# Kernel tuning notes

Hardware: AMD Instinct MI355X
Metric: run time of the kernel (lower is better)

## Reference

```python
import jax, jax.numpy as jnp
import numpy as np


def _lstm_cell(x, h, c, Wih, Whh, b):
    # torch gate order: input, forget, cell(g), output
    gates = x @ Wih.T + h @ Whh.T + b  # [B, 4H]
    i, f, g, o = jnp.split(gates, 4, axis=-1)
    i = jax.nn.sigmoid(i)
    f = jax.nn.sigmoid(f)
    g = jnp.tanh(g)
    o = jax.nn.sigmoid(o)
    c = f * c + i * g
    return o * jnp.tanh(c), c


def setup_inputs() -> dict:
    key = jax.random.key(0)
    ks = jax.random.split(key, 20)
    B, Te, Td, X, H = 4096, 168, 24, 8, 64
    s = 0.1  # weight scale for numerical sanity in the AR sampling loop
    return {
        "enc_x": jax.random.normal(ks[0], (B, Te, X), jnp.float32),
        "enc_z": jax.random.uniform(ks[1], (B, Te, 1), jnp.float32),
        "dec_x": jax.random.normal(ks[2], (B, Td, X - 1), jnp.float32),
        "v": jax.random.uniform(ks[3], (B, 1, 1), jnp.float32) + 0.5,  # positive scale
        "eps": jax.random.normal(ks[4], (B, Td, 1), jnp.float32),
        "W_ih0": s * jax.random.normal(ks[5], (4 * H, X), jnp.float32),
        "W_hh0": s * jax.random.normal(ks[6], (4 * H, H), jnp.float32),
        "b0": s * jax.random.normal(ks[7], (4 * H,), jnp.float32),
        "W_ih1": s * jax.random.normal(ks[8], (4 * H, H), jnp.float32),
        "W_hh1": s * jax.random.normal(ks[9], (4 * H, H), jnp.float32),
        "b1": s * jax.random.normal(ks[10], (4 * H,), jnp.float32),
        "W_ih2": s * jax.random.normal(ks[11], (4 * H, H), jnp.float32),
        "W_hh2": s * jax.random.normal(ks[12], (4 * H, H), jnp.float32),
        "b2": s * jax.random.normal(ks[13], (4 * H,), jnp.float32),
        "w_m": s * jax.random.normal(ks[14], (H, 1), jnp.float32),
        "b_m": jnp.zeros((1,), jnp.float32),
        "w_a": s * jax.random.normal(ks[15], (H, 1), jnp.float32),
        "b_a": jnp.zeros((1,), jnp.float32),
    }


def reference(enc_x, enc_z, dec_x, v, eps,
              W_ih0, W_hh0, b0, W_ih1, W_hh1, b1, W_ih2, W_hh2, b2,
              w_m, b_m, w_a, b_a):
    B = enc_x.shape[0]
    H = W_hh0.shape[1]

    def step3(x, h, c):
        h0, c0 = _lstm_cell(x, h[0], c[0], W_ih0, W_hh0, b0)
        h1, c1 = _lstm_cell(h0, h[1], c[1], W_ih1, W_hh1, b1)
        h2, c2 = _lstm_cell(h1, h[2], c[2], W_ih2, W_hh2, b2)
        return (h0, h1, h2), (c0, c1, c2), h2

    z0 = jnp.zeros((B, H), enc_x.dtype)
    h = (z0, z0, z0)
    c = (z0, z0, z0)

    # ---- encoder: 3-layer LSTM over Te steps ----
    def enc_step(carry, x_t):
        h, c = carry
        h, c, _ = step3(x_t, h, c)
        return (h, c), None

    (h, c), _ = jax.lax.scan(enc_step, (h, c), jnp.swapaxes(enc_x, 0, 1))

    vf = v[:, 0, :]                 # [B, 1]
    z = enc_z[:, -1, :] / vf        # [B, 1]

    def dec_step(carry, inp):
        h, c, z = carry
        x_t, e_t = inp              # [B, X-1], [B, 1]
        x = jnp.concatenate([z, x_t], axis=-1)   # [B, X]
        h, c, o = step3(x, h, c)
        m = (o @ w_m + b_m) * vf                  # Gaussian mean, rescaled
        a = jax.nn.softplus(o @ w_a + b_a) * vf   # Gaussian std, rescaled
        zs = m + a * e_t                          # reparameterized sample
        return (h, c, zs / vf), zs

    xs = (jnp.swapaxes(dec_x, 0, 1), jnp.swapaxes(eps, 0, 1))
    _, Z = jax.lax.scan(dec_step, (h, c, z), xs)  # [Td, B, 1]
    return jnp.swapaxes(Z, 0, 1)                  # [B, Td, 1]
```

## Files before the change

kernel.cpp:

```cpp
#include <hip/hip_runtime.h>
#include <math.h>

#define B_TOT 4096
#define TE 168
#define TD 24
#define NWG 256
#define HSTR 72

typedef _Float16 f16;
typedef __attribute__((ext_vector_type(8))) _Float16 f16x8;
typedef __attribute__((ext_vector_type(4))) float f32x4;

#define SCL_S (-1.4426950408889634f)
#define SCL_G (2.885390081777927f)

__global__ __launch_bounds__(256) void pack_kernel(
    const float* __restrict__ Wih0, const float* __restrict__ Whh0,
    const float* __restrict__ Wih1, const float* __restrict__ Whh1,
    const float* __restrict__ Wih2, const float* __restrict__ Whh2,
    f16* __restrict__ pk)
{
    int idx = blockIdx.x * 256 + threadIdx.x;
    int j = idx & 7;
    int t = idx >> 3;
    int ln = t & 63; t >>= 6;
    int c  = t & 3;  t >>= 2;
    int q  = t & 3;  t >>= 2;
    int l  = t % 3;
    int w  = t / 3;
    int row = q * 64 + w * 16 + (ln & 15);
    int k   = c * 32 + ((ln >> 4) << 3) + j;
    float val = 0.f;
    if (l == 0) {
        if (k < 8)                 val = Wih0[row * 8 + k];
        else if (k >= 32 && k < 96) val = Whh0[row * 64 + (k - 32)];
    } else if (l == 1) {
        val = (k < 64) ? Wih1[row * 64 + k] : Whh1[row * 64 + (k - 64)];
    } else {
        val = (k < 64) ? Wih2[row * 64 + k] : Whh2[row * 64 + (k - 64)];
    }
    const float sc = (q == 2) ? SCL_G : SCL_S;
    pk[idx] = (f16)(val * sc);
}

__device__ __forceinline__ float softplusf(float x) { return fmaxf(x, 0.f) + log1pf(__expf(-fabsf(x))); }

__global__ __launch_bounds__(256, 1) void lstm_kernel(
    const float* __restrict__ enc_x, const float* __restrict__ enc_z,
    const float* __restrict__ dec_x, const float* __restrict__ v,
    const float* __restrict__ eps,   const f16* __restrict__ pk,
    const float* __restrict__ b0, const float* __restrict__ b1,
    const float* __restrict__ b2,
    const float* __restrict__ w_m, const float* __restrict__ b_m,
    const float* __restrict__ w_a, const float* __restrict__ b_a,
    float* __restrict__ out)
{
    const int tid  = threadIdx.x;
    const int lane = tid & 63;
    const int wv   = tid >> 6;
    const int bg   = blockIdx.x * 16;
    const int m16  = lane & 15;
    const int quad = lane >> 4;

    __shared__ f16  hbuf[2][3][16][HSTR];
    __shared__ f16  xbuf[16][32];
    __shared__ float zbuf[16];

    {
        uint* hz = (uint*)&hbuf[0][0][0][0];
        const int HW = 2 * 3 * 16 * HSTR / 2;
        for (int i = tid; i < HW; i += 256) hz[i] = 0u;
        ((uint*)&xbuf[0][0])[tid] = 0u;
    }

    f16x8 wgt[3][4][4];
#pragma unroll
    for (int l = 0; l < 3; ++l)
#pragma unroll
        for (int q = 0; q < 4; ++q)
#pragma unroll
            for (int c = 0; c < 4; ++c) {
                if (l == 0 && c == 3) continue;
                size_t off = (((((size_t)wv * 3 + l) * 4 + q) * 4 + c) * 64 + lane) * 8;
                wgt[l][q][c] = *(const f16x8*)(pk + off);
            }

    const int hid_self = wv * 16 + m16;
    f32x4 bsp[3][4];
#pragma unroll
    for (int q = 0; q < 4; ++q) {
        const float sc = (q == 2) ? SCL_G : SCL_S;
        float v0 = b0[q * 64 + hid_self] * sc;
        float v1 = b1[q * 64 + hid_self] * sc;
        float v2 = b2[q * 64 + hid_self] * sc;
        bsp[0][q] = (f32x4){v0, v0, v0, v0};
        bsp[1][q] = (f32x4){v1, v1, v1, v1};
        bsp[2][q] = (f32x4){v2, v2, v2, v2};
    }

    f16* hb = &hbuf[0][0][0][0];
    const int aoff = m16 * HSTR + quad * 8;
    float cst[3][4] = {};

#define HBASE(pp, l) (hb + ((pp) * 3 + (l)) * (16 * HSTR))
#define MFMA16(af, bf, cf) __builtin_amdgcn_mfma_f32_16x16x32_f16(af, bf, cf, 0, 0, 0)

#define MM_F(P, aptr, l, c)                                                   \
    {                                                                         \
        f16x8 af = *(const f16x8*)(aptr);                                     \
        P##0 = MFMA16(af, wgt[l][0][c], bsp[l][0]);                           \
        P##1 = MFMA16(af, wgt[l][1][c], bsp[l][1]);                           \
        P##2 = MFMA16(af, wgt[l][2][c], bsp[l][2]);                           \
        P##3 = MFMA16(af, wgt[l][3][c], bsp[l][3]);                           \
    }
#define MM(P, aptr, l, c)                                                     \
    {                                                                         \
        f16x8 af = *(const f16x8*)(aptr);                                     \
        P##0 = MFMA16(af, wgt[l][0][c], P##0);                                \
        P##1 = MFMA16(af, wgt[l][1][c], P##1);                                \
        P##2 = MFMA16(af, wgt[l][2][c], P##2);                                \
        P##3 = MFMA16(af, wgt[l][3][c], P##3);                                \
    }

#define CELL(P, l, PP)                                                        \
    {                                                                         \
        f16* hw = HBASE(PP, l) + hid_self;                                    \
        _Pragma("unroll")                                                     \
        for (int r = 0; r < 4; ++r) {                                         \
            float iv = __builtin_amdgcn_rcpf(1.f + __builtin_amdgcn_exp2f(P##0[r])); \
            float fv = __builtin_amdgcn_rcpf(1.f + __builtin_amdgcn_exp2f(P##1[r])); \
            float gv = fmaf(-2.f, __builtin_amdgcn_rcpf(1.f + __builtin_amdgcn_exp2f(P##2[r])), 1.f); \
            float ov = __builtin_amdgcn_rcpf(1.f + __builtin_amdgcn_exp2f(P##3[r])); \
            float cn = fmaf(fv, cst[l][r], iv * gv);                          \
            cst[l][r] = cn;                                                   \
            float tc = fmaf(-2.f, __builtin_amdgcn_rcpf(1.f + __builtin_amdgcn_exp2f(cn * SCL_G)), 1.f); \
            hw[(quad * 4 + r) * HSTR] = (f16)(ov * tc);                       \
        }                                                                     \
    }

    const int  mS   = tid >> 3, kS = tid & 7;
    const bool isst = tid < 128;

#define ENC_STEP(PP, t)                                                       \
    {                                                                         \
        __syncthreads();                       \
        f32x4 ac0, ac1, ac2, ac3, bc0, bc1, bc2, bc3;                         \
        MM_F(ac, &xbuf[0][0] + m16 * 32 + quad * 8, 0, 0);                    \
        MM_F(bc, HBASE(1 - (PP), 1) + aoff, 1, 2);                            \
        MM(ac, HBASE(1 - (PP), 0) + aoff, 0, 1);                              \
        MM(bc, HBASE(1 - (PP), 1) + aoff + 32, 1, 3);                         \
        MM(ac, HBASE(1 - (PP), 0) + aoff + 32, 0, 2);                         \
        CELL(ac, 0, PP);                                                      \
        __syncthreads();                    \
        if (isst && (t) + 1 < TE) {                                           \
            xbuf[mS][kS] = (f16)xpre;                                         \
            if ((t) + 2 < TE)                                                 \
                xpre = enc_x[((size_t)(bg + mS) * TE + (t) + 2) * 8 + kS];    \
        }                                                                     \
        MM_F(ac, HBASE(1 - (PP), 2) + aoff, 2, 2);                            \
        MM(bc, HBASE(PP, 0) + aoff, 1, 0);                                    \
        MM(ac, HBASE(1 - (PP), 2) + aoff + 32, 2, 3);                         \
        MM(bc, HBASE(PP, 0) + aoff + 32, 1, 1);                               \
        CELL(bc, 1, PP);                                                      \
        __syncthreads();                               \
        MM(ac, HBASE(PP, 1) + aoff, 2, 0);                                    \
        MM(ac, HBASE(PP, 1) + aoff + 32, 2, 1);                               \
        CELL(ac, 2, PP);                                                      \
    }

    __syncthreads();

    float xpre = 0.f;
    if (isst) {
        xbuf[mS][kS] = (f16)enc_x[((size_t)(bg + mS) * TE + 0) * 8 + kS];
        xpre = enc_x[((size_t)(bg + mS) * TE + 1) * 8 + kS];
    }
    for (int t = 0; t < TE; t += 2) {
        ENC_STEP(0, t)
        ENC_STEP(1, t + 1)
    }

    const int   mH = tid >> 4;
    const float vf = v[bg + mH];
    float wmr[4], war[4];
#pragma unroll
    for (int r = 0; r < 4; ++r) {
        wmr[r] = w_m[(tid & 15) + 16 * r];
        war[r] = w_a[(tid & 15) + 16 * r];
    }
    const float bmv = b_m[0], bav = b_a[0];
    if ((tid & 15) == 0) zbuf[mH] = enc_z[(size_t)(bg + mH) * TE + (TE - 1)] / vf;

#define DEC_STEP(PP, t)                                                       \
    {                                                                         \
        __syncthreads();                        \
        if (isst) {                                                           \
            float xv = (kS == 0) ? zbuf[mS]                                   \
                                 : dec_x[((size_t)(bg + mS) * TD + (t)) * 7 + (kS - 1)]; \
            xbuf[mS][kS] = (f16)xv;                                           \
        }                                                                     \
        __syncthreads();                                \
        f32x4 ac0, ac1, ac2, ac3, bc0, bc1, bc2, bc3;                         \
        MM_F(ac, &xbuf[0][0] + m16 * 32 + quad * 8, 0, 0);                    \
        MM_F(bc, HBASE(1 - (PP), 1) + aoff, 1, 2);                            \
        MM(ac, HBASE(1 - (PP), 0) + aoff, 0, 1);                              \
        MM(bc, HBASE(1 - (PP), 1) + aoff + 32, 1, 3);                         \
        MM(ac, HBASE(1 - (PP), 0) + aoff + 32, 0, 2);                         \
        CELL(ac, 0, PP);                                                      \
        __syncthreads();                                               \
        MM_F(ac, HBASE(1 - (PP), 2) + aoff, 2, 2);                            \
        MM(bc, HBASE(PP, 0) + aoff, 1, 0);                                    \
        MM(ac, HBASE(1 - (PP), 2) + aoff + 32, 2, 3);                         \
        MM(bc, HBASE(PP, 0) + aoff + 32, 1, 1);                               \
        CELL(bc, 1, PP);                                                      \
        __syncthreads();                                               \
        MM(ac, HBASE(PP, 1) + aoff, 2, 0);                                    \
        MM(ac, HBASE(PP, 1) + aoff + 32, 2, 1);                               \
        CELL(ac, 2, PP);                                                      \
        __syncthreads();                               \
        {                                                                     \
            float sm = 0.f, sa = 0.f;                                         \
            const f16* h2p = HBASE(PP, 2) + mH * HSTR;                        \
            _Pragma("unroll")                                                 \
            for (int r = 0; r < 4; ++r) {                                     \
                float hv = (float)h2p[(tid & 15) + 16 * r];                   \
                sm += hv * wmr[r];                                            \
                sa += hv * war[r];                                            \
            }                                                                 \
            _Pragma("unroll")                                                 \
            for (int off = 1; off < 16; off <<= 1) {                          \
                sm += __shfl_xor(sm, off, 64);                                \
                sa += __shfl_xor(sa, off, 64);                                \
            }                                                                 \
            if ((tid & 15) == 0) {                                            \
                float mo  = (sm + bmv) * vf;                                  \
                float ao  = softplusf(sa + bav) * vf;                         \
                float zsv = mo + ao * eps[(size_t)(bg + mH) * TD + (t)];      \
                out[(size_t)(bg + mH) * TD + (t)] = zsv;                      \
                zbuf[mH] = zsv / vf;                                          \
            }                                                                 \
        }                                                                     \
    }

    for (int t = 0; t < TD; t += 2) {
        DEC_STEP(0, t)
        DEC_STEP(1, t + 1)
    }

#undef HBASE
#undef MFMA16
#undef MM_F
#undef MM
#undef CELL
#undef ENC_STEP
#undef DEC_STEP
}

extern "C" void kernel_launch(void* const* d_in, const int* in_sizes, int n_in,
                              void* d_out, int out_size, void* d_ws, size_t ws_size,
                              hipStream_t stream) {
    const float* enc_x = (const float*)d_in[0];
    const float* enc_z = (const float*)d_in[1];
    const float* dec_x = (const float*)d_in[2];
    const float* v     = (const float*)d_in[3];
    const float* eps   = (const float*)d_in[4];
    const float* Wih0  = (const float*)d_in[5];
    const float* Whh0  = (const float*)d_in[6];
    const float* b0    = (const float*)d_in[7];
    const float* Wih1  = (const float*)d_in[8];
    const float* Whh1  = (const float*)d_in[9];
    const float* b1    = (const float*)d_in[10];
    const float* Wih2  = (const float*)d_in[11];
    const float* Whh2  = (const float*)d_in[12];
    const float* b2    = (const float*)d_in[13];
    const float* w_m   = (const float*)d_in[14];
    const float* b_m   = (const float*)d_in[15];
    const float* w_a   = (const float*)d_in[16];
    const float* b_a   = (const float*)d_in[17];
    float* out = (float*)d_out;
    f16*   pk  = (f16*)d_ws;

    pack_kernel<<<384, 256, 0, stream>>>(Wih0, Whh0, Wih1, Whh1, Wih2, Whh2, pk);
    lstm_kernel<<<NWG, 256, 0, stream>>>(enc_x, enc_z, dec_x, v, eps, pk,
                                         b0, b1, b2, w_m, b_m, w_a, b_a, out);
}
```

Before: 364.9 us.

## Wavefront-pipeline encoder layers across timesteps and merge sigmoid/tanh reciprocals

The encoder now runs as a diagonal wavefront. In each round, layer 0 handles step t, layer 1 step t-1 and layer 2 step t-2, so a single barrier per round replaces three per step. Prologue and epilogue rounds fill and drain the pipeline, x is double-buffered, and the decoder's buffer parity is adjusted to match the skewed hidden-state layout. The cell math also combines pairs of reciprocals (i·g and o·tanh(c)) into one rcp each, which shortens the transcendental chain. The trade-off is more live accumulator registers per round and possible overflow in the merged products for large gate pre-activations.

```diff
diff --git a/kernel.cpp b/kernel.cpp
--- a/kernel.cpp
+++ b/kernel.cpp
@@ -63,14 +63,15 @@
     const int quad = lane >> 4;
 
     __shared__ f16  hbuf[2][3][16][HSTR];
-    __shared__ f16  xbuf[16][32];
+    __shared__ f16  xbuf[2][16][32];
     __shared__ float zbuf[16];
 
     {
         uint* hz = (uint*)&hbuf[0][0][0][0];
         const int HW = 2 * 3 * 16 * HSTR / 2;
         for (int i = tid; i < HW; i += 256) hz[i] = 0u;
-        ((uint*)&xbuf[0][0])[tid] = 0u;
+        uint* xz = (uint*)&xbuf[0][0][0];
+        for (int i = tid; i < 512; i += 256) xz[i] = 0u;
     }
 
     f16x8 wgt[3][4][4];
@@ -127,58 +128,70 @@
         f16* hw = HBASE(PP, l) + hid_self;                                    \
         _Pragma("unroll")                                                     \
         for (int r = 0; r < 4; ++r) {                                         \
-            float iv = __builtin_amdgcn_rcpf(1.f + __builtin_amdgcn_exp2f(P##0[r])); \
-            float fv = __builtin_amdgcn_rcpf(1.f + __builtin_amdgcn_exp2f(P##1[r])); \
-            float gv = fmaf(-2.f, __builtin_amdgcn_rcpf(1.f + __builtin_amdgcn_exp2f(P##2[r])), 1.f); \
-            float ov = __builtin_amdgcn_rcpf(1.f + __builtin_amdgcn_exp2f(P##3[r])); \
-            float cn = fmaf(fv, cst[l][r], iv * gv);                          \
+            float Ei = __builtin_amdgcn_exp2f(P##0[r]);                       \
+            float Ef = __builtin_amdgcn_exp2f(P##1[r]);                       \
+            float Eg = __builtin_amdgcn_exp2f(P##2[r]);                       \
+            float Eo = __builtin_amdgcn_exp2f(P##3[r]);                       \
+            float fv  = __builtin_amdgcn_rcpf(1.f + Ef);                      \
+            float Rig = __builtin_amdgcn_rcpf((1.f + Ei) * (1.f + Eg));       \
+            float cn  = fmaf(fv, cst[l][r], (Eg - 1.f) * Rig);                \
             cst[l][r] = cn;                                                   \
-            float tc = fmaf(-2.f, __builtin_amdgcn_rcpf(1.f + __builtin_amdgcn_exp2f(cn * SCL_G)), 1.f); \
-            hw[(quad * 4 + r) * HSTR] = (f16)(ov * tc);                       \
+            float Ec  = __builtin_amdgcn_exp2f(cn * SCL_G);                   \
+            float Roc = __builtin_amdgcn_rcpf((1.f + Eo) * (1.f + Ec));       \
+            hw[(quad * 4 + r) * HSTR] = (f16)((Ec - 1.f) * Roc);              \
         }                                                                     \
     }
 
     const int  mS   = tid >> 3, kS = tid & 7;
     const bool isst = tid < 128;
 
-#define ENC_STEP(PP, t)                                                       \
-    {                                                                         \
-        __syncthreads();                       \
-        f32x4 ac0, ac1, ac2, ac3, bc0, bc1, bc2, bc3;                         \
-        MM_F(ac, &xbuf[0][0] + m16 * 32 + quad * 8, 0, 0);                    \
-        MM_F(bc, HBASE(1 - (PP), 1) + aoff, 1, 2);                            \
-        MM(ac, HBASE(1 - (PP), 0) + aoff, 0, 1);                              \
-        MM(bc, HBASE(1 - (PP), 1) + aoff + 32, 1, 3);                         \
-        MM(ac, HBASE(1 - (PP), 0) + aoff + 32, 0, 2);                         \
-        CELL(ac, 0, PP);                                                      \
-        __syncthreads();                    \
-        if (isst && (t) + 1 < TE) {                                           \
-            xbuf[mS][kS] = (f16)xpre;                                         \
-            if ((t) + 2 < TE)                                                 \
-                xpre = enc_x[((size_t)(bg + mS) * TE + (t) + 2) * 8 + kS];    \
-        }                                                                     \
-        MM_F(ac, HBASE(1 - (PP), 2) + aoff, 2, 2);                            \
-        MM(bc, HBASE(PP, 0) + aoff, 1, 0);                                    \
-        MM(ac, HBASE(1 - (PP), 2) + aoff + 32, 2, 3);                         \
-        MM(bc, HBASE(PP, 0) + aoff + 32, 1, 1);                               \
-        CELL(bc, 1, PP);                                                      \
-        __syncthreads();                               \
-        MM(ac, HBASE(PP, 1) + aoff, 2, 0);                                    \
-        MM(ac, HBASE(PP, 1) + aoff + 32, 2, 1);                               \
-        CELL(ac, 2, PP);                                                      \
+#define ROUND(PP, D0, D1, D2, DS, DP, T0)                                     \
+    {                                                                         \
+        __syncthreads();                                                      \
+        f32x4 a00, a01, a02, a03, a10, a11, a12, a13, a20, a21, a22, a23;     \
+        if (D0) {                                                             \
+            MM_F(a0, &xbuf[PP][0][0] + m16 * 32 + quad * 8, 0, 0);            \
+            MM(a0, HBASE(1 - (PP), 0) + aoff,      0, 1);                     \
+            MM(a0, HBASE(1 - (PP), 0) + aoff + 32, 0, 2);                     \
+        }                                                                     \
+        if (D1) {                                                             \
+            MM_F(a1, HBASE(1 - (PP), 0) + aoff,      1, 0);                   \
+            MM(a1, HBASE(1 - (PP), 0) + aoff + 32, 1, 1);                     \
+            MM(a1, HBASE(1 - (PP), 1) + aoff,      1, 2);                     \
+            MM(a1, HBASE(1 - (PP), 1) + aoff + 32, 1, 3);                     \
+        }                                                                     \
+        if (D2) {                                                             \
+            MM_F(a2, HBASE(1 - (PP), 1) + aoff,      2, 0);                   \
+            MM(a2, HBASE(1 - (PP), 1) + aoff + 32, 2, 1);                     \
+            MM(a2, HBASE(1 - (PP), 2) + aoff,      2, 2);                     \
+            MM(a2, HBASE(1 - (PP), 2) + aoff + 32, 2, 3);                     \
+        }                                                                     \
+        if (DS && isst) {                                                     \
+            xbuf[1 - (PP)][mS][kS] = (f16)xpre;                               \
+            if (DP) xpre = enc_x[((size_t)(bg + mS) * TE + (T0) + 2) * 8 + kS]; \
+        }                                                                     \
+        if (D0) CELL(a0, 0, PP);                                              \
+        if (D1) CELL(a1, 1, PP);                                              \
+        if (D2) CELL(a2, 2, PP);                                              \
     }
 
     __syncthreads();
 
     float xpre = 0.f;
     if (isst) {
-        xbuf[mS][kS] = (f16)enc_x[((size_t)(bg + mS) * TE + 0) * 8 + kS];
+        xbuf[0][mS][kS] = (f16)enc_x[((size_t)(bg + mS) * TE + 0) * 8 + kS];
         xpre = enc_x[((size_t)(bg + mS) * TE + 1) * 8 + kS];
     }
-    for (int t = 0; t < TE; t += 2) {
-        ENC_STEP(0, t)
-        ENC_STEP(1, t + 1)
-    }
+    ROUND(0, 1, 0, 0, 1, 1, 0)
+    ROUND(1, 1, 1, 0, 1, 1, 1)
+    for (int t = 2; t < 166; t += 2) {
+        ROUND(0, 1, 1, 1, 1, 1, t)
+        ROUND(1, 1, 1, 1, 1, 1, t + 1)
+    }
+    ROUND(0, 1, 1, 1, 1, 0, 166)
+    ROUND(1, 1, 1, 1, 0, 0, 167)
+    ROUND(0, 0, 1, 1, 0, 0, 168)
+    ROUND(1, 0, 0, 1, 0, 0, 169)
 
     const int   mH = tid >> 4;
     const float vf = v[bg + mH];
@@ -191,36 +204,36 @@
     const float bmv = b_m[0], bav = b_a[0];
     if ((tid & 15) == 0) zbuf[mH] = enc_z[(size_t)(bg + mH) * TE + (TE - 1)] / vf;
 
-#define DEC_STEP(PP, t)                                                       \
-    {                                                                         \
-        __syncthreads();                        \
+#define DEC_STEP(PA, t)                                                       \
+    {                                                                         \
+        __syncthreads();                      \
         if (isst) {                                                           \
             float xv = (kS == 0) ? zbuf[mS]                                   \
                                  : dec_x[((size_t)(bg + mS) * TD + (t)) * 7 + (kS - 1)]; \
-            xbuf[mS][kS] = (f16)xv;                                           \
-        }                                                                     \
+            xbuf[PA][mS][kS] = (f16)xv;                                       \
+        }                                                                     \
+        __syncthreads();                                       \
+        f32x4 ac0, ac1, ac2, ac3, bc0, bc1, bc2, bc3;                         \
+        MM_F(ac, &xbuf[PA][0][0] + m16 * 32 + quad * 8, 0, 0);                \
+        MM_F(bc, HBASE(PA, 1) + aoff,      1, 2);                             \
+        MM(ac, HBASE(1 - (PA), 0) + aoff,      0, 1);                         \
+        MM(bc, HBASE(PA, 1) + aoff + 32, 1, 3);                               \
+        MM(ac, HBASE(1 - (PA), 0) + aoff + 32, 0, 2);                         \
+        CELL(ac, 0, PA);                                                      \
+        __syncthreads();                                  \
+        MM_F(ac, HBASE(1 - (PA), 2) + aoff,      2, 2);                       \
+        MM(bc, HBASE(PA, 0) + aoff,      1, 0);                               \
+        MM(ac, HBASE(1 - (PA), 2) + aoff + 32, 2, 3);                         \
+        MM(bc, HBASE(PA, 0) + aoff + 32, 1, 1);                               \
+        CELL(bc, 1, 1 - (PA));                                                \
         __syncthreads();                                \
-        f32x4 ac0, ac1, ac2, ac3, bc0, bc1, bc2, bc3;                         \
-        MM_F(ac, &xbuf[0][0] + m16 * 32 + quad * 8, 0, 0);                    \
-        MM_F(bc, HBASE(1 - (PP), 1) + aoff, 1, 2);                            \
-        MM(ac, HBASE(1 - (PP), 0) + aoff, 0, 1);                              \
-        MM(bc, HBASE(1 - (PP), 1) + aoff + 32, 1, 3);                         \
-        MM(ac, HBASE(1 - (PP), 0) + aoff + 32, 0, 2);                         \
-        CELL(ac, 0, PP);                                                      \
-        __syncthreads();                                               \
-        MM_F(ac, HBASE(1 - (PP), 2) + aoff, 2, 2);                            \
-        MM(bc, HBASE(PP, 0) + aoff, 1, 0);                                    \
-        MM(ac, HBASE(1 - (PP), 2) + aoff + 32, 2, 3);                         \
-        MM(bc, HBASE(PP, 0) + aoff + 32, 1, 1);                               \
-        CELL(bc, 1, PP);                                                      \
-        __syncthreads();                                               \
-        MM(ac, HBASE(PP, 1) + aoff, 2, 0);                                    \
-        MM(ac, HBASE(PP, 1) + aoff + 32, 2, 1);                               \
-        CELL(ac, 2, PP);                                                      \
-        __syncthreads();                               \
+        MM(ac, HBASE(1 - (PA), 1) + aoff,      2, 0);                         \
+        MM(ac, HBASE(1 - (PA), 1) + aoff + 32, 2, 1);                         \
+        CELL(ac, 2, PA);                                                      \
+        __syncthreads();                                  \
         {                                                                     \
             float sm = 0.f, sa = 0.f;                                         \
-            const f16* h2p = HBASE(PP, 2) + mH * HSTR;                        \
+            const f16* h2p = HBASE(PA, 2) + mH * HSTR;                        \
             _Pragma("unroll")                                                 \
             for (int r = 0; r < 4; ++r) {                                     \
                 float hv = (float)h2p[(tid & 15) + 16 * r];                   \
@@ -252,7 +265,7 @@
 #undef MM_F
 #undef MM
 #undef CELL
-#undef ENC_STEP
+#undef ROUND
 #undef DEC_STEP
 }
 
```

After: 339.1 us. -7.1%, faster.
